# Optimization experiments

Measured on AMD Instinct MI355X. Metric: run time of the kernel, lower is better.

The kernel has to match this reference:

```python
import jax, jax.numpy as jnp
import numpy as np

# ---- Cl(4,1) Cayley table (conformal GA: metric +,+,+,+,-) ----
_METRIC = (1.0, 1.0, 1.0, 1.0, -1.0)

def _reorder_sign(a, b):
    # sign from counting swaps to bring blade product to canonical order
    a >>= 1
    s = 0
    while a:
        s += bin(a & b).count("1")
        a >>= 1
    return -1.0 if (s & 1) else 1.0

def _build_cayley():
    C = np.zeros((32, 32, 32), dtype=np.float32)
    for a in range(32):
        for b in range(32):
            s = _reorder_sign(a, b)
            common = a & b
            for i in range(5):
                if (common >> i) & 1:
                    s *= _METRIC[i]
            C[a, b, a ^ b] += s
    return C

CAYLEY = _build_cayley()  # [32,32,32]; out_k = sum_ij C[i,j,k] x_i y_j

EPS = 1e-8

def normalize_cl41(x):
    n = jnp.sqrt(jnp.sum(x * x, axis=-1, keepdims=True))
    return x / (n + EPS)


def setup_inputs() -> dict:
    key = jax.random.key(0)
    k_x, k_wi, k_bi, k_wo, k_bo = jax.random.split(key, 5)
    B, S, D, H = 64, 2048, 6, 8
    x = jax.random.normal(k_x, (B, S, D), dtype=jnp.float32)
    W_in = jax.random.normal(k_wi, (D, H * 32), dtype=jnp.float32) * (1.0 / np.sqrt(D))
    b_in = jax.random.normal(k_bi, (H * 32,), dtype=jnp.float32) * 0.01
    W_out = jax.random.normal(k_wo, (H * 32, 32), dtype=jnp.float32) * (1.0 / np.sqrt(H * 32))
    b_out = jax.random.normal(k_bo, (32,), dtype=jnp.float32) * 0.01
    return {"x": x, "W_in": W_in, "b_in": b_in, "W_out": W_out, "b_out": b_out}


def reference(x, W_in, b_in, W_out, b_out):
    B, S, D = x.shape
    H = W_in.shape[1] // 32
    C = jnp.asarray(CAYLEY)
    # project inputs to per-channel multivectors: (B,S,H,32)
    u = (x @ W_in + b_in).reshape(B, S, H, 32)
    # initial rotor state: identity (scalar blade = 1)
    psi0 = jnp.zeros((B, H, 32), dtype=x.dtype).at[..., 0].set(1.0)

    def step(psi, u_t):  # u_t: (B,H,32)
        delta = normalize_cl41(u_t.at[..., 0].add(1.0))
        psi = normalize_cl41(jnp.einsum("bhi,bhj,ijk->bhk", delta, psi, C))
        return psi, psi

    _, psi_seq = jax.lax.scan(step, psi0, jnp.swapaxes(u, 0, 1))  # (S,B,H,32)
    out = normalize_cl41(psi_seq.reshape(S, B, H * 32) @ W_out + b_out)  # (S,B,32)
    return jnp.swapaxes(out, 0, 1)  # (B,S,32)
```

## Files before the change

kernel.cpp:

```cpp
#include <hip/hip_runtime.h>
#include <hip/hip_bf16.h>
#include <stdint.h>

#define BB 64
#define SS 2048
#define DD 6
#define HH 8
#define NCH 512
#define CHUNKS 256
#define LCH 8

typedef unsigned short ushort_t;
typedef __attribute__((ext_vector_type(8))) __bf16 bf16x8;
typedef __attribute__((ext_vector_type(4))) float f32x4;

struct SignTab { float s[32][32]; };

constexpr int popc5_c(unsigned v) {
    int c = 0;
    for (int i = 0; i < 5; ++i) c += (v >> i) & 1u;
    return c;
}

constexpr SignTab make_signs() {
    SignTab t{};
    for (int a = 0; a < 32; ++a) {
        for (int b = 0; b < 32; ++b) {
            int cnt = 0;
            unsigned aa = ((unsigned)a) >> 1;
            while (aa) { cnt += popc5_c(aa & (unsigned)b); aa >>= 1; }
            if ((a & b) & 16) cnt += 1;
            t.s[a][b] = (cnt & 1) ? -1.0f : 1.0f;
        }
    }
    return t;
}

constexpr SignTab SGN = make_signs();

__device__ __forceinline__ void gp_cl41(const float* __restrict__ a,
                                        const float* __restrict__ b,
                                        float* __restrict__ o) {
#pragma unroll
    for (int k = 0; k < 32; ++k) o[k] = 0.0f;
#pragma unroll
    for (int i = 0; i < 32; ++i) {
#pragma unroll
        for (int k = 0; k < 32; ++k) {
            o[k] = fmaf(SGN.s[i][i ^ k] * a[i], b[i ^ k], o[k]);
        }
    }
}

__device__ __forceinline__ float sumsq32(const float* v) {
    float n0 = 0.f, n1 = 0.f, n2 = 0.f, n3 = 0.f;
#pragma unroll
    for (int k = 0; k < 32; k += 4) {
        n0 = fmaf(v[k+0], v[k+0], n0);
        n1 = fmaf(v[k+1], v[k+1], n1);
        n2 = fmaf(v[k+2], v[k+2], n2);
        n3 = fmaf(v[k+3], v[k+3], n3);
    }
    return (n0 + n1) + (n2 + n3);
}

__device__ __forceinline__ float rsq(float n) {
    return __builtin_amdgcn_rsqf(n);
}

__device__ __forceinline__ uint32_t f2bf_rne(float f) {
    uint32_t u = __float_as_uint(f);
    return (u + 0x7FFFu + ((u >> 16) & 1u)) >> 16;
}

__device__ __forceinline__ uint32_t packh2(float a, float b) {
    union { _Float16 h[2]; uint32_t u; } t;
    t.h[0] = (_Float16)a; t.h[1] = (_Float16)b;
    return t.u;
}
__device__ __forceinline__ float h2lo(uint32_t u) {
    union { uint32_t u32; _Float16 h[2]; } t; t.u32 = u; return (float)t.h[0];
}
__device__ __forceinline__ float h2hi(uint32_t u) {
    union { uint32_t u32; _Float16 h[2]; } t; t.u32 = u; return (float)t.h[1];
}

__global__ __launch_bounds__(256) void k_local(
        const float* __restrict__ x, const float* __restrict__ W_in,
        const float* __restrict__ b_in, ushort_t* __restrict__ psi_loc,
        float* __restrict__ Tbuf) {
    __shared__ float4 sW4[8][57];
    for (int idx = threadIdx.x; idx < 8 * 56; idx += 256) {
        int h = idx / 56, r = idx % 56;
        float4 v;
        if (r < 48) {
            int d = r / 8, j4 = r % 8;
            const float* p = W_in + d * 256 + h * 32 + 4 * j4;
            v = make_float4(p[0], p[1], p[2], p[3]);
        } else {
            const float* p = b_in + h * 32 + 4 * (r - 48);
            v = make_float4(p[0], p[1], p[2], p[3]);
        }
        sW4[h][r] = v;
    }
    __syncthreads();

    int tid = blockIdx.x * 256 + threadIdx.x;
    int c  = tid >> 9;
    int bh = tid & 511;
    int b = bh >> 3, h = bh & 7;

    float4 bias4[8];
#pragma unroll
    for (int j4 = 0; j4 < 8; ++j4) bias4[j4] = sW4[h][48 + j4];

    float p[32];
#pragma unroll
    for (int k = 0; k < 32; ++k) p[k] = 0.f;
    p[0] = 1.f;

    const float* xrow = x + ((size_t)b * SS + (size_t)c * LCH) * DD;
    ushort_t* psi_base = psi_loc + (((size_t)b * SS + (size_t)c * LCH) * HH + h) * 32;

#pragma unroll 1
    for (int pr = 0; pr < LCH / 2; ++pr) {
        float xv[12];
#pragma unroll
        for (int d = 0; d < 6; ++d) {
            float2 t2 = *(const float2*)(xrow + 2 * d);
            xv[2 * d] = t2.x; xv[2 * d + 1] = t2.y;
        }
        xrow += 12;
        float x0[6], x1[6];
#pragma unroll
        for (int d = 0; d < 6; ++d) { x0[d] = xv[d]; x1[d] = xv[6 + d]; }

        float dl0[32], dl1[32];
#pragma unroll
        for (int j4 = 0; j4 < 8; ++j4) {
            float4 bv = bias4[j4];
            dl0[4*j4+0] = bv.x; dl0[4*j4+1] = bv.y; dl0[4*j4+2] = bv.z; dl0[4*j4+3] = bv.w;
            dl1[4*j4+0] = bv.x; dl1[4*j4+1] = bv.y; dl1[4*j4+2] = bv.z; dl1[4*j4+3] = bv.w;
        }
#pragma unroll
        for (int d = 0; d < 6; ++d) {
            float a0 = x0[d], a1 = x1[d];
#pragma unroll
            for (int j4 = 0; j4 < 8; ++j4) {
                float4 w = sW4[h][d * 8 + j4];
                dl0[4*j4+0] = fmaf(a0, w.x, dl0[4*j4+0]);
                dl0[4*j4+1] = fmaf(a0, w.y, dl0[4*j4+1]);
                dl0[4*j4+2] = fmaf(a0, w.z, dl0[4*j4+2]);
                dl0[4*j4+3] = fmaf(a0, w.w, dl0[4*j4+3]);
                dl1[4*j4+0] = fmaf(a1, w.x, dl1[4*j4+0]);
                dl1[4*j4+1] = fmaf(a1, w.y, dl1[4*j4+1]);
                dl1[4*j4+2] = fmaf(a1, w.z, dl1[4*j4+2]);
                dl1[4*j4+3] = fmaf(a1, w.w, dl1[4*j4+3]);
            }
        }
        dl0[0] += 1.0f;
        dl1[0] += 1.0f;

        float o[32];
        gp_cl41(dl0, p, o);
        {
            float inv = rsq(sumsq32(o));
            ushort_t* dst = psi_base + (size_t)(2 * pr) * HH * 32;
            uint32_t pk[16];
#pragma unroll
            for (int m = 0; m < 16; ++m)
                pk[m] = packh2(o[2*m] * inv, o[2*m+1] * inv);
            uint4* d4 = (uint4*)dst;
#pragma unroll
            for (int m = 0; m < 4; ++m)
                d4[m] = make_uint4(pk[4*m], pk[4*m+1], pk[4*m+2], pk[4*m+3]);
        }
        gp_cl41(dl1, o, p);
        {
            float inv = rsq(sumsq32(p));
            ushort_t* dst = psi_base + (size_t)(2 * pr + 1) * HH * 32;
            uint32_t pk[16];
#pragma unroll
            for (int m = 0; m < 16; ++m)
                pk[m] = packh2(p[2*m] * inv, p[2*m+1] * inv);
            uint4* d4 = (uint4*)dst;
#pragma unroll
            for (int m = 0; m < 4; ++m)
                d4[m] = make_uint4(pk[4*m], pk[4*m+1], pk[4*m+2], pk[4*m+3]);
        }
    }

    float inv = rsq(sumsq32(p));
    float* dst = Tbuf + ((size_t)bh * CHUNKS + c) * 32;
#pragma unroll
    for (int k = 0; k < 32; ++k) dst[k] = p[k] * inv;
}

__global__ __launch_bounds__(256) void k_scan_totals(
        const float* __restrict__ Tbuf, float* __restrict__ Ebuf) {
    __shared__ float sT[CHUNKS][33];
    int chain = blockIdx.x;
    int c = threadIdx.x;

    float v[32];
    const float* src = Tbuf + ((size_t)chain * CHUNKS + c) * 32;
#pragma unroll
    for (int k = 0; k < 32; ++k) { v[k] = src[k]; sT[c][k] = v[k]; }
    __syncthreads();

#pragma unroll 1
    for (int off = 1; off < CHUNKS; off <<= 1) {
        float w[32];
        bool act = (c >= off);
        if (act) {
#pragma unroll
            for (int k = 0; k < 32; ++k) w[k] = sT[c - off][k];
        }
        __syncthreads();
        if (act) {
            float o[32];
            gp_cl41(v, w, o);
            float inv = rsq(sumsq32(o));
#pragma unroll
            for (int k = 0; k < 32; ++k) { v[k] = o[k] * inv; sT[c][k] = v[k]; }
        }
        __syncthreads();
    }

    float* dst = Ebuf + (size_t)chain * CHUNKS * 32;
    if (c == 0) {
#pragma unroll
        for (int k = 0; k < 32; ++k) dst[k] = (k == 0) ? 1.f : 0.f;
    }
    if (c < CHUNKS - 1) {
        float* d2 = dst + (size_t)(c + 1) * 32;
#pragma unroll
        for (int k = 0; k < 32; ++k) d2[k] = v[k];
    }
}

__global__ __launch_bounds__(256) void k_fixup_proj(
        const ushort_t* __restrict__ psi_loc, const float* __restrict__ Ebuf,
        const float* __restrict__ W_out, const float* __restrict__ b_out,
        float* __restrict__ out) {
    int lane = threadIdx.x & 63;
    int wv = threadIdx.x >> 6;
    int q = lane >> 4;
    int n0 = lane & 15;

    bf16x8 Bf[2][8];
#pragma unroll
    for (int nt = 0; nt < 2; ++nt)
#pragma unroll
        for (int kk = 0; kk < 8; ++kk) {
            union { ushort_t u[8]; bf16x8 v; } tmp;
#pragma unroll
            for (int j = 0; j < 8; ++j)
                tmp.u[j] = (ushort_t)f2bf_rne(W_out[(kk * 32 + q * 8 + j) * 32 + nt * 16 + n0]);
            Bf[nt][kk] = tmp.v;
        }
    float bn0 = b_out[n0], bn1 = b_out[16 + n0];

    __shared__ ushort_t psiT[4][16][264];

#pragma unroll 1
    for (int tile = blockIdx.x * 4 + wv; tile < 8192; tile += 2048) {
        int rr0 = tile * 16;
        int b = rr0 >> 11;
        int s0 = rr0 & 2047;

        __syncthreads();

#pragma unroll
        for (int pp = 0; pp < 2; ++pp) {
            int row_local = pp * 8 + (lane >> 3);
            int h = lane & 7;
            int s = s0 + row_local;
            int c = s >> 3;
            int bh = b * 8 + h;

            float a[32], w[32], o[32];
            const uint4* pl = (const uint4*)(psi_loc +
                    (((size_t)b * SS + s) * HH + h) * 32);
#pragma unroll
            for (int m = 0; m < 4; ++m) {
                uint4 t4 = pl[m];
                uint32_t uu[4] = { t4.x, t4.y, t4.z, t4.w };
#pragma unroll
                for (int z = 0; z < 4; ++z) {
                    a[8*m + 2*z]     = h2lo(uu[z]);
                    a[8*m + 2*z + 1] = h2hi(uu[z]);
                }
            }
            const float* e = Ebuf + ((size_t)bh * CHUNKS + c) * 32;
#pragma unroll
            for (int k = 0; k < 32; ++k) w[k] = e[k];

            gp_cl41(a, w, o);
            float inv = rsq(sumsq32(o));

            uint32_t pk[16];
#pragma unroll
            for (int m = 0; m < 16; ++m)
                pk[m] = f2bf_rne(o[2*m] * inv) | (f2bf_rne(o[2*m+1] * inv) << 16);
            uint4* dst = (uint4*)&psiT[wv][row_local][h * 32];
#pragma unroll
            for (int m = 0; m < 4; ++m)
                dst[m] = make_uint4(pk[4*m], pk[4*m+1], pk[4*m+2], pk[4*m+3]);
        }

        __syncthreads();

        f32x4 acc0 = {0.f, 0.f, 0.f, 0.f};
        f32x4 acc1 = {0.f, 0.f, 0.f, 0.f};
#pragma unroll
        for (int kk = 0; kk < 8; ++kk) {
            bf16x8 af = *(const bf16x8*)&psiT[wv][n0][kk * 32 + q * 8];
            acc0 = __builtin_amdgcn_mfma_f32_16x16x32_bf16(af, Bf[0][kk], acc0, 0, 0, 0);
            acc1 = __builtin_amdgcn_mfma_f32_16x16x32_bf16(af, Bf[1][kk], acc1, 0, 0, 0);
        }

        float c0[4], c1[4], ss[4];
#pragma unroll
        for (int i = 0; i < 4; ++i) {
            c0[i] = acc0[i] + bn0;
            c1[i] = acc1[i] + bn1;
            ss[i] = c0[i] * c0[i] + c1[i] * c1[i];
        }
#pragma unroll
        for (int m = 1; m < 16; m <<= 1) {
#pragma unroll
            for (int i = 0; i < 4; ++i) ss[i] += __shfl_xor(ss[i], m);
        }
#pragma unroll
        for (int i = 0; i < 4; ++i) {
            float inv = rsq(ss[i]);
            int row = rr0 + q * 4 + i;
            out[(size_t)row * 32 + n0]      = c0[i] * inv;
            out[(size_t)row * 32 + 16 + n0] = c1[i] * inv;
        }
    }
}

extern "C" void kernel_launch(void* const* d_in, const int* in_sizes, int n_in,
                              void* d_out, int out_size, void* d_ws, size_t ws_size,
                              hipStream_t stream) {
    const float* x     = (const float*)d_in[0];
    const float* W_in  = (const float*)d_in[1];
    const float* b_in  = (const float*)d_in[2];
    const float* W_out = (const float*)d_in[3];
    const float* b_out = (const float*)d_in[4];
    float* out = (float*)d_out;

    char* ws = (char*)d_ws;
    float* Tbuf = (float*)ws;
    float* Ebuf = Tbuf;
    ushort_t* psi = (ushort_t*)(ws + (size_t)16 * 1024 * 1024);

    k_local      <<<512, 256, 0, stream>>>(x, W_in, b_in, psi, Tbuf);
    k_scan_totals<<<512, 256, 0, stream>>>(Tbuf, Ebuf);
    k_fixup_proj <<<512, 256, 0, stream>>>(psi, Ebuf, W_out, b_out, out);
}
```

Before: 197.5 us.

## Pair chunks in scan, prefetch x in local pass, one tile per wave in fixup

The chunk-total scan now has each of 128 threads combine two adjacent chunk totals first. It runs a 7-step Hillis-Steele scan instead of 8 steps over 256 threads, then reconstructs the odd-chunk prefix with one extra geometric product. The local pass loads the next pair of x rows with float4 loads one iteration ahead. The fixup/projection kernel drops its grid-stride loop and launches 2048 blocks, each wave handling a single 16-row tile. The workspace layout is also reordered. Together these aim to cut scan latency and sync steps and to improve occupancy and latency hiding, at the cost of extra per-thread products and more block launches.

```diff
diff --git a/kernel.cpp b/kernel.cpp
--- a/kernel.cpp
+++ b/kernel.cpp
@@ -83,6 +83,31 @@
 }
 __device__ __forceinline__ float h2hi(uint32_t u) {
     union { uint32_t u32; _Float16 h[2]; } t; t.u32 = u; return (float)t.h[1];
+}
+
+__device__ __forceinline__ void pack_store16(ushort_t* dst, const float* v, float scale) {
+    uint32_t pk[16];
+#pragma unroll
+    for (int m = 0; m < 16; ++m)
+        pk[m] = packh2(v[2*m] * scale, v[2*m+1] * scale);
+    uint4* d4 = (uint4*)dst;
+#pragma unroll
+    for (int m = 0; m < 4; ++m)
+        d4[m] = make_uint4(pk[4*m], pk[4*m+1], pk[4*m+2], pk[4*m+3]);
+}
+
+__device__ __forceinline__ void load_unpack16(const ushort_t* src, float* v) {
+    const uint4* s4 = (const uint4*)src;
+#pragma unroll
+    for (int m = 0; m < 4; ++m) {
+        uint4 t4 = s4[m];
+        uint32_t uu[4] = { t4.x, t4.y, t4.z, t4.w };
+#pragma unroll
+        for (int z = 0; z < 4; ++z) {
+            v[8*m + 2*z]     = h2lo(uu[z]);
+            v[8*m + 2*z + 1] = h2hi(uu[z]);
+        }
+    }
 }
 
 __global__ __launch_bounds__(256) void k_local(
@@ -122,18 +147,30 @@
     const float* xrow = x + ((size_t)b * SS + (size_t)c * LCH) * DD;
     ushort_t* psi_base = psi_loc + (((size_t)b * SS + (size_t)c * LCH) * HH + h) * 32;
 
+    float xc[12];
+    {
+        const float4* xp = (const float4*)xrow;
+#pragma unroll
+        for (int m = 0; m < 3; ++m) {
+            float4 t4 = xp[m];
+            xc[4*m+0] = t4.x; xc[4*m+1] = t4.y; xc[4*m+2] = t4.z; xc[4*m+3] = t4.w;
+        }
+    }
+
 #pragma unroll 1
     for (int pr = 0; pr < LCH / 2; ++pr) {
-        float xv[12];
-#pragma unroll
-        for (int d = 0; d < 6; ++d) {
-            float2 t2 = *(const float2*)(xrow + 2 * d);
-            xv[2 * d] = t2.x; xv[2 * d + 1] = t2.y;
-        }
-        xrow += 12;
         float x0[6], x1[6];
 #pragma unroll
-        for (int d = 0; d < 6; ++d) { x0[d] = xv[d]; x1[d] = xv[6 + d]; }
+        for (int d = 0; d < 6; ++d) { x0[d] = xc[d]; x1[d] = xc[6 + d]; }
+
+        if (pr < LCH / 2 - 1) {
+            const float4* xp = (const float4*)(xrow + (pr + 1) * 12);
+#pragma unroll
+            for (int m = 0; m < 3; ++m) {
+                float4 t4 = xp[m];
+                xc[4*m+0] = t4.x; xc[4*m+1] = t4.y; xc[4*m+2] = t4.z; xc[4*m+3] = t4.w;
+            }
+        }
 
         float dl0[32], dl1[32];
 #pragma unroll
@@ -163,31 +200,9 @@
 
         float o[32];
         gp_cl41(dl0, p, o);
-        {
-            float inv = rsq(sumsq32(o));
-            ushort_t* dst = psi_base + (size_t)(2 * pr) * HH * 32;
-            uint32_t pk[16];
-#pragma unroll
-            for (int m = 0; m < 16; ++m)
-                pk[m] = packh2(o[2*m] * inv, o[2*m+1] * inv);
-            uint4* d4 = (uint4*)dst;
-#pragma unroll
-            for (int m = 0; m < 4; ++m)
-                d4[m] = make_uint4(pk[4*m], pk[4*m+1], pk[4*m+2], pk[4*m+3]);
-        }
+        pack_store16(psi_base + (size_t)(2 * pr) * HH * 32, o, rsq(sumsq32(o)));
         gp_cl41(dl1, o, p);
-        {
-            float inv = rsq(sumsq32(p));
-            ushort_t* dst = psi_base + (size_t)(2 * pr + 1) * HH * 32;
-            uint32_t pk[16];
-#pragma unroll
-            for (int m = 0; m < 16; ++m)
-                pk[m] = packh2(p[2*m] * inv, p[2*m+1] * inv);
-            uint4* d4 = (uint4*)dst;
-#pragma unroll
-            for (int m = 0; m < 4; ++m)
-                d4[m] = make_uint4(pk[4*m], pk[4*m+1], pk[4*m+2], pk[4*m+3]);
-        }
+        pack_store16(psi_base + (size_t)(2 * pr + 1) * HH * 32, p, rsq(sumsq32(p)));
     }
 
     float inv = rsq(sumsq32(p));
@@ -196,25 +211,38 @@
     for (int k = 0; k < 32; ++k) dst[k] = p[k] * inv;
 }
 
-__global__ __launch_bounds__(256) void k_scan_totals(
+__global__ __launch_bounds__(128) void k_scan_totals(
         const float* __restrict__ Tbuf, float* __restrict__ Ebuf) {
-    __shared__ float sT[CHUNKS][33];
+    __shared__ float sT[128][33];
     int chain = blockIdx.x;
-    int c = threadIdx.x;
+    int pp = threadIdx.x;
+
+    float t0[32], t1[32];
+    {
+        const float* s0 = Tbuf + ((size_t)chain * CHUNKS + 2 * pp) * 32;
+#pragma unroll
+        for (int k = 0; k < 32; ++k) t0[k] = s0[k];
+#pragma unroll
+        for (int k = 0; k < 32; ++k) t1[k] = s0[32 + k];
+    }
 
     float v[32];
-    const float* src = Tbuf + ((size_t)chain * CHUNKS + c) * 32;
-#pragma unroll
-    for (int k = 0; k < 32; ++k) { v[k] = src[k]; sT[c][k] = v[k]; }
+    {
+        float o[32];
+        gp_cl41(t1, t0, o);
+        float inv = rsq(sumsq32(o));
+#pragma unroll
+        for (int k = 0; k < 32; ++k) { v[k] = o[k] * inv; sT[pp][k] = v[k]; }
+    }
     __syncthreads();
 
 #pragma unroll 1
-    for (int off = 1; off < CHUNKS; off <<= 1) {
+    for (int off = 1; off < 128; off <<= 1) {
         float w[32];
-        bool act = (c >= off);
+        bool act = (pp >= off);
         if (act) {
 #pragma unroll
-            for (int k = 0; k < 32; ++k) w[k] = sT[c - off][k];
+            for (int k = 0; k < 32; ++k) w[k] = sT[pp - off][k];
         }
         __syncthreads();
         if (act) {
@@ -222,21 +250,28 @@
             gp_cl41(v, w, o);
             float inv = rsq(sumsq32(o));
 #pragma unroll
-            for (int k = 0; k < 32; ++k) { v[k] = o[k] * inv; sT[c][k] = v[k]; }
+            for (int k = 0; k < 32; ++k) { v[k] = o[k] * inv; sT[pp][k] = v[k]; }
         }
         __syncthreads();
     }
 
-    float* dst = Ebuf + (size_t)chain * CHUNKS * 32;
-    if (c == 0) {
-#pragma unroll
-        for (int k = 0; k < 32; ++k) dst[k] = (k == 0) ? 1.f : 0.f;
-    }
-    if (c < CHUNKS - 1) {
-        float* d2 = dst + (size_t)(c + 1) * 32;
-#pragma unroll
-        for (int k = 0; k < 32; ++k) d2[k] = v[k];
-    }
+    float e0[32];
+    if (pp == 0) {
+#pragma unroll
+        for (int k = 0; k < 32; ++k) e0[k] = (k == 0) ? 1.f : 0.f;
+    } else {
+#pragma unroll
+        for (int k = 0; k < 32; ++k) e0[k] = sT[pp - 1][k];
+    }
+    float e1[32];
+    gp_cl41(t0, e0, e1);
+    float inv1 = rsq(sumsq32(e1));
+
+    float* d0 = Ebuf + ((size_t)chain * CHUNKS + 2 * pp) * 32;
+#pragma unroll
+    for (int k = 0; k < 32; ++k) d0[k] = e0[k];
+#pragma unroll
+    for (int k = 0; k < 32; ++k) d0[32 + k] = e1[k] * inv1;
 }
 
 __global__ __launch_bounds__(256) void k_fixup_proj(
@@ -263,82 +298,67 @@
 
     __shared__ ushort_t psiT[4][16][264];
 
-#pragma unroll 1
-    for (int tile = blockIdx.x * 4 + wv; tile < 8192; tile += 2048) {
-        int rr0 = tile * 16;
-        int b = rr0 >> 11;
-        int s0 = rr0 & 2047;
-
-        __syncthreads();
-
-#pragma unroll
-        for (int pp = 0; pp < 2; ++pp) {
-            int row_local = pp * 8 + (lane >> 3);
-            int h = lane & 7;
-            int s = s0 + row_local;
-            int c = s >> 3;
-            int bh = b * 8 + h;
-
-            float a[32], w[32], o[32];
-            const uint4* pl = (const uint4*)(psi_loc +
-                    (((size_t)b * SS + s) * HH + h) * 32);
-#pragma unroll
-            for (int m = 0; m < 4; ++m) {
-                uint4 t4 = pl[m];
-                uint32_t uu[4] = { t4.x, t4.y, t4.z, t4.w };
-#pragma unroll
-                for (int z = 0; z < 4; ++z) {
-                    a[8*m + 2*z]     = h2lo(uu[z]);
-                    a[8*m + 2*z + 1] = h2hi(uu[z]);
-                }
-            }
-            const float* e = Ebuf + ((size_t)bh * CHUNKS + c) * 32;
-#pragma unroll
-            for (int k = 0; k < 32; ++k) w[k] = e[k];
-
-            gp_cl41(a, w, o);
-            float inv = rsq(sumsq32(o));
-
-            uint32_t pk[16];
-#pragma unroll
-            for (int m = 0; m < 16; ++m)
-                pk[m] = f2bf_rne(o[2*m] * inv) | (f2bf_rne(o[2*m+1] * inv) << 16);
-            uint4* dst = (uint4*)&psiT[wv][row_local][h * 32];
-#pragma unroll
-            for (int m = 0; m < 4; ++m)
-                dst[m] = make_uint4(pk[4*m], pk[4*m+1], pk[4*m+2], pk[4*m+3]);
-        }
-
-        __syncthreads();
-
-        f32x4 acc0 = {0.f, 0.f, 0.f, 0.f};
-        f32x4 acc1 = {0.f, 0.f, 0.f, 0.f};
-#pragma unroll
-        for (int kk = 0; kk < 8; ++kk) {
-            bf16x8 af = *(const bf16x8*)&psiT[wv][n0][kk * 32 + q * 8];
-            acc0 = __builtin_amdgcn_mfma_f32_16x16x32_bf16(af, Bf[0][kk], acc0, 0, 0, 0);
-            acc1 = __builtin_amdgcn_mfma_f32_16x16x32_bf16(af, Bf[1][kk], acc1, 0, 0, 0);
-        }
-
-        float c0[4], c1[4], ss[4];
-#pragma unroll
-        for (int i = 0; i < 4; ++i) {
-            c0[i] = acc0[i] + bn0;
-            c1[i] = acc1[i] + bn1;
-            ss[i] = c0[i] * c0[i] + c1[i] * c1[i];
-        }
-#pragma unroll
-        for (int m = 1; m < 16; m <<= 1) {
-#pragma unroll
-            for (int i = 0; i < 4; ++i) ss[i] += __shfl_xor(ss[i], m);
-        }
-#pragma unroll
-        for (int i = 0; i < 4; ++i) {
-            float inv = rsq(ss[i]);
-            int row = rr0 + q * 4 + i;
-            out[(size_t)row * 32 + n0]      = c0[i] * inv;
-            out[(size_t)row * 32 + 16 + n0] = c1[i] * inv;
-        }
+    int tile = blockIdx.x * 4 + wv;
+    int rr0 = tile * 16;
+    int b = rr0 >> 11;
+    int s0 = rr0 & 2047;
+
+#pragma unroll
+    for (int pp = 0; pp < 2; ++pp) {
+        int row_local = pp * 8 + (lane >> 3);
+        int h = lane & 7;
+        int s = s0 + row_local;
+        int c = s >> 3;
+        int bh = b * 8 + h;
+
+        float a[32], w[32], o[32];
+        load_unpack16(psi_loc + (((size_t)b * SS + s) * HH + h) * 32, a);
+        const float* e = Ebuf + ((size_t)bh * CHUNKS + c) * 32;
+#pragma unroll
+        for (int k = 0; k < 32; ++k) w[k] = e[k];
+
+        gp_cl41(a, w, o);
+        float inv = rsq(sumsq32(o));
+
+        uint32_t pk[16];
+#pragma unroll
+        for (int m = 0; m < 16; ++m)
+            pk[m] = f2bf_rne(o[2*m] * inv) | (f2bf_rne(o[2*m+1] * inv) << 16);
+        uint4* dst = (uint4*)&psiT[wv][row_local][h * 32];
+#pragma unroll
+        for (int m = 0; m < 4; ++m)
+            dst[m] = make_uint4(pk[4*m], pk[4*m+1], pk[4*m+2], pk[4*m+3]);
+    }
+
+    __syncthreads();
+
+    f32x4 acc0 = {0.f, 0.f, 0.f, 0.f};
+    f32x4 acc1 = {0.f, 0.f, 0.f, 0.f};
+#pragma unroll
+    for (int kk = 0; kk < 8; ++kk) {
+        bf16x8 af = *(const bf16x8*)&psiT[wv][n0][kk * 32 + q * 8];
+        acc0 = __builtin_amdgcn_mfma_f32_16x16x32_bf16(af, Bf[0][kk], acc0, 0, 0, 0);
+        acc1 = __builtin_amdgcn_mfma_f32_16x16x32_bf16(af, Bf[1][kk], acc1, 0, 0, 0);
+    }
+
+    float c0[4], c1[4], ss[4];
+#pragma unroll
+    for (int i = 0; i < 4; ++i) {
+        c0[i] = acc0[i] + bn0;
+        c1[i] = acc1[i] + bn1;
+        ss[i] = c0[i] * c0[i] + c1[i] * c1[i];
+    }
+#pragma unroll
+    for (int m = 1; m < 16; m <<= 1) {
+#pragma unroll
+        for (int i = 0; i < 4; ++i) ss[i] += __shfl_xor(ss[i], m);
+    }
+#pragma unroll
+    for (int i = 0; i < 4; ++i) {
+        float inv = rsq(ss[i]);
+        int row = rr0 + q * 4 + i;
+        out[(size_t)row * 32 + n0]      = c0[i] * inv;
+        out[(size_t)row * 32 + 16 + n0] = c1[i] * inv;
     }
 }
 
@@ -353,11 +373,11 @@
     float* out = (float*)d_out;
 
     char* ws = (char*)d_ws;
-    float* Tbuf = (float*)ws;
+    ushort_t* psi  = (ushort_t*)ws;
+    float* Tbuf = (float*)(ws + (size_t)64 * 1024 * 1024);
     float* Ebuf = Tbuf;
-    ushort_t* psi = (ushort_t*)(ws + (size_t)16 * 1024 * 1024);
-
-    k_local      <<<512, 256, 0, stream>>>(x, W_in, b_in, psi, Tbuf);
-    k_scan_totals<<<512, 256, 0, stream>>>(Tbuf, Ebuf);
-    k_fixup_proj <<<512, 256, 0, stream>>>(psi, Ebuf, W_out, b_out, out);
-}
+
+    k_local      <<< 512, 256, 0, stream>>>(x, W_in, b_in, psi, Tbuf);
+    k_scan_totals<<< 512, 128, 0, stream>>>(Tbuf, Ebuf);
+    k_fixup_proj <<<2048, 256, 0, stream>>>(psi, Ebuf, W_out, b_out, out);
+}
```

Result: slower. 203.7 us (+3.1%).
